# Kernel optimization log

Hardware: AMD Instinct MI355X
Metric: run time of the kernel (lower is better)

Reference implementation:

```python
import jax, jax.numpy as jnp
import numpy as np

OUT = 128
TYPES = [("author", 100000, 128), ("paper", 250000, 256), ("venue", 25000, 64),
         ("institution", 50000, 128), ("field", 75000, 64), ("term", 150000, 128)]


def setup_inputs() -> dict:
    key = jax.random.key(0)
    inp = {}
    for i, (name, n, f_in) in enumerate(TYPES):
        kx, kw, kb = jax.random.split(jax.random.fold_in(key, i), 3)
        inp[f"x_{name}"] = jax.random.normal(kx, (n, f_in), dtype=jnp.float32)
        # kaiming_uniform default init of torch Linear: bound = 1/sqrt(fan_in)
        bound = 1.0 / np.sqrt(f_in)
        inp[f"W_{name}"] = jax.random.uniform(kw, (OUT, f_in), dtype=jnp.float32, minval=-bound, maxval=bound)
        inp[f"b_{name}"] = jax.random.uniform(kb, (OUT,), dtype=jnp.float32, minval=-bound, maxval=bound)
    return inp


def reference(x_author, x_paper, x_venue, x_institution, x_field, x_term,
              W_author, b_author, W_paper, b_paper, W_venue, b_venue,
              W_institution, b_institution, W_field, b_field, W_term, b_term):
    # Per-type independent Linear: y_k = x_k @ W_k^T + b_k (grouped GEMM)
    def lin(x, W, b):
        return jnp.einsum('nf,of->no', x, W) + b
    return (lin(x_author, W_author, b_author),
            lin(x_paper, W_paper, b_paper),
            lin(x_venue, W_venue, b_venue),
            lin(x_institution, W_institution, b_institution),
            lin(x_field, W_field, b_field),
            lin(x_term, W_term, b_term))
```

## Files before the change

kernel.cpp:

```cpp
#include <hip/hip_runtime.h>

typedef __bf16 bf16x4 __attribute__((ext_vector_type(4)));
typedef __bf16 bf16x8 __attribute__((ext_vector_type(8)));
typedef float  f32x4  __attribute__((ext_vector_type(4)));

struct KArgs {
    const float* x[6];
    const float* W[6];
    const float* b[6];
    float*       out[6];
    int nrows[6];
    int blk0[7];
};

template<int FIN>
__device__ __forceinline__ void run_type(
    const float* __restrict__ x, const float* __restrict__ W,
    const float* __restrict__ bias, float* __restrict__ out,
    int nrows, int c0, int c1, __bf16* __restrict__ Alds)
{
    constexpr int KS    = (FIN < 128) ? FIN : 128;
    constexpr int NSLAB = FIN / KS;
    constexpr int NC    = FIN / 32;
    constexpr int CPS   = KS / 32;
    constexpr int UPT   = KS / 16;
    constexpr int BATCH = (UPT > 4) ? 4 : UPT;

    const int tid  = threadIdx.x;
    const int lane = tid & 63;
    const int wave = tid >> 6;
    const int l15  = lane & 15;
    const int lq   = lane >> 4;

    bf16x8 Wf[NC][2];
    f32x4  bv[2];
    #pragma unroll
    for (int t = 0; t < 2; ++t) {
        const int o = wave * 32 + t * 16 + l15;
        #pragma unroll
        for (int c = 0; c < NC; ++c) {
            const int k0 = c * 32 + lq * 8;
            const f32x4 w0 = *(const f32x4*)(W + (size_t)o * FIN + k0);
            const f32x4 w1 = *(const f32x4*)(W + (size_t)o * FIN + k0 + 4);
            bf16x8 f;
            f[0] = (__bf16)w0[0]; f[1] = (__bf16)w0[1];
            f[2] = (__bf16)w0[2]; f[3] = (__bf16)w0[3];
            f[4] = (__bf16)w1[0]; f[5] = (__bf16)w1[1];
            f[6] = (__bf16)w1[2]; f[7] = (__bf16)w1[3];
            Wf[c][t] = f;
        }
        bv[t] = *(const f32x4*)(bias + wave * 32 + t * 16 + lq * 4);
    }

    for (int chunk = c0; chunk < c1; ++chunk) {
        const int row0 = chunk * 64;
        f32x4 acc[4][2] = {};

        #pragma unroll
        for (int slab = 0; slab < NSLAB; ++slab) {
            __syncthreads();

            #pragma unroll
            for (int b0 = 0; b0 < UPT; b0 += BATCH) {
                f32x4 tmp[BATCH];
                #pragma unroll
                for (int i = 0; i < BATCH; ++i) {
                    const int u  = tid + (b0 + i) * 256;
                    const int r  = u / (KS / 4);
                    const int kq = u % (KS / 4);
                    int gr = row0 + r;
                    if (gr >= nrows) gr = nrows - 1;
                    tmp[i] = __builtin_nontemporal_load(
                        (const f32x4*)(x + (size_t)gr * FIN + slab * KS + kq * 4));
                }
                #pragma unroll
                for (int i = 0; i < BATCH; ++i) {
                    const int u  = tid + (b0 + i) * 256;
                    const int r  = u / (KS / 4);
                    const int kq = u % (KS / 4);
                    bf16x4 bq;
                    bq[0] = (__bf16)tmp[i][0]; bq[1] = (__bf16)tmp[i][1];
                    bq[2] = (__bf16)tmp[i][2]; bq[3] = (__bf16)tmp[i][3];
                    const int byte = (r * KS * 2 + kq * 8) ^ ((r & 7) << 4);
                    *(bf16x4*)((char*)Alds + byte) = bq;
                }
            }
            __syncthreads();

            #pragma unroll
            for (int nt = 0; nt < 4; ++nt) {
                const int row = nt * 16 + l15;
                #pragma unroll
                for (int c = 0; c < CPS; ++c) {
                    const int byte = (row * KS * 2 + c * 64 + lq * 16) ^ ((row & 7) << 4);
                    const bf16x8 xf = *(const bf16x8*)((char*)Alds + byte);
                    acc[nt][0] = __builtin_amdgcn_mfma_f32_16x16x32_bf16(
                        Wf[slab * CPS + c][0], xf, acc[nt][0], 0, 0, 0);
                    acc[nt][1] = __builtin_amdgcn_mfma_f32_16x16x32_bf16(
                        Wf[slab * CPS + c][1], xf, acc[nt][1], 0, 0, 0);
                }
            }
        }

        #pragma unroll
        for (int nt = 0; nt < 4; ++nt) {
            const int xrow = row0 + nt * 16 + l15;
            if (xrow < nrows) {
                #pragma unroll
                for (int t = 0; t < 2; ++t) {
                    const f32x4 v = acc[nt][t] + bv[t];
                    __builtin_nontemporal_store(v,
                        (f32x4*)(out + (size_t)xrow * 128 + wave * 32 + t * 16 + lq * 4));
                }
            }
        }
    }
}

__global__ __launch_bounds__(256) void hetero_fused_kern(KArgs A)
{
    __shared__ __bf16 Alds[64 * 128];

    int ty = 0;
    const int bid = blockIdx.x;
    while (ty < 5 && bid >= A.blk0[ty + 1]) ++ty;
    const int lb = bid - A.blk0[ty];
    const int nb = A.blk0[ty + 1] - A.blk0[ty];

    const int nrows  = A.nrows[ty];
    const int chunks = (nrows + 63) >> 6;
    const int c0 = (int)(((long)chunks * lb) / nb);
    const int c1 = (int)(((long)chunks * (lb + 1)) / nb);
    if (c0 >= c1) return;

    switch (ty) {
        case 0: run_type<128>(A.x[0], A.W[0], A.b[0], A.out[0], nrows, c0, c1, Alds); break;
        case 1: run_type<256>(A.x[1], A.W[1], A.b[1], A.out[1], nrows, c0, c1, Alds); break;
        case 2: run_type< 64>(A.x[2], A.W[2], A.b[2], A.out[2], nrows, c0, c1, Alds); break;
        case 3: run_type<128>(A.x[3], A.W[3], A.b[3], A.out[3], nrows, c0, c1, Alds); break;
        case 4: run_type< 64>(A.x[4], A.W[4], A.b[4], A.out[4], nrows, c0, c1, Alds); break;
        case 5: run_type<128>(A.x[5], A.W[5], A.b[5], A.out[5], nrows, c0, c1, Alds); break;
    }
}

extern "C" void kernel_launch(void* const* d_in, const int* in_sizes, int n_in,
                              void* d_out, int out_size, void* d_ws, size_t ws_size,
                              hipStream_t stream)
{
    float* out = (float*)d_out;
    KArgs A;
    const int   nrows[6] = {100000, 250000, 25000, 50000, 75000, 150000};
    const long  ooff[6]  = {0L, 12800000L, 44800000L, 48000000L, 54400000L, 64000000L};
    const int   blk0[7]  = {0, 273, 1297, 1348, 1485, 1639, 2048};
    for (int t = 0; t < 6; ++t) {
        A.x[t]     = (const float*)d_in[3 * t + 0];
        A.W[t]     = (const float*)d_in[3 * t + 1];
        A.b[t]     = (const float*)d_in[3 * t + 2];
        A.out[t]   = out + ooff[t];
        A.nrows[t] = nrows[t];
    }
    for (int i = 0; i < 7; ++i) A.blk0[i] = blk0[i];

    hetero_fused_kern<<<2048, 256, 0, stream>>>(A);
}
```

Baseline: 169.2 us.

## Load activations directly into MFMA fragments, dropping LDS staging and barriers

Replaces the shared-memory staging of activation tiles with direct per-lane global loads converted straight into bf16 MFMA operands, removing both __syncthreads per slab. Each wave now covers 16 rows by 64 output columns, so a block handles 32-row chunks and every weight fragment set doubles in registers. This aims to cut LDS traffic and barrier stalls and to add an occupancy hint. In exchange, each x row is fetched by two waves, global access is less coalesced per instruction, and register pressure rises for the 256-wide type.

```diff
diff --git a/kernel.cpp b/kernel.cpp
--- a/kernel.cpp
+++ b/kernel.cpp
@@ -1,6 +1,5 @@
 #include <hip/hip_runtime.h>
 
-typedef __bf16 bf16x4 __attribute__((ext_vector_type(4)));
 typedef __bf16 bf16x8 __attribute__((ext_vector_type(8)));
 typedef float  f32x4  __attribute__((ext_vector_type(4)));
 
@@ -17,31 +16,26 @@
 __device__ __forceinline__ void run_type(
     const float* __restrict__ x, const float* __restrict__ W,
     const float* __restrict__ bias, float* __restrict__ out,
-    int nrows, int c0, int c1, __bf16* __restrict__ Alds)
+    int nrows, int c0, int c1)
 {
-    constexpr int KS    = (FIN < 128) ? FIN : 128;
-    constexpr int NSLAB = FIN / KS;
-    constexpr int NC    = FIN / 32;
-    constexpr int CPS   = KS / 32;
-    constexpr int UPT   = KS / 16;
-    constexpr int BATCH = (UPT > 4) ? 4 : UPT;
+    constexpr int NC = FIN / 32;
 
-    const int tid  = threadIdx.x;
-    const int lane = tid & 63;
-    const int wave = tid >> 6;
-    const int l15  = lane & 15;
-    const int lq   = lane >> 4;
+    const int tid     = threadIdx.x;
+    const int lane    = tid & 63;
+    const int wave    = tid >> 6;
+    const int l15     = lane & 15;
+    const int lq      = lane >> 4;
+    const int rowgrp  = wave >> 1;
+    const int colbase = (wave & 1) * 64;
 
-    bf16x8 Wf[NC][2];
-    f32x4  bv[2];
+    bf16x8 Wf[NC][4];
     #pragma unroll
-    for (int t = 0; t < 2; ++t) {
-        const int o = wave * 32 + t * 16 + l15;
+    for (int t = 0; t < 4; ++t) {
+        const int o = colbase + t * 16 + l15;
         #pragma unroll
         for (int c = 0; c < NC; ++c) {
-            const int k0 = c * 32 + lq * 8;
-            const f32x4 w0 = *(const f32x4*)(W + (size_t)o * FIN + k0);
-            const f32x4 w1 = *(const f32x4*)(W + (size_t)o * FIN + k0 + 4);
+            const f32x4 w0 = *(const f32x4*)(W + (size_t)o * FIN + c * 32 + lq * 8);
+            const f32x4 w1 = *(const f32x4*)(W + (size_t)o * FIN + c * 32 + lq * 8 + 4);
             bf16x8 f;
             f[0] = (__bf16)w0[0]; f[1] = (__bf16)w0[1];
             f[2] = (__bf16)w0[2]; f[3] = (__bf16)w0[3];
@@ -49,78 +43,44 @@
             f[6] = (__bf16)w1[2]; f[7] = (__bf16)w1[3];
             Wf[c][t] = f;
         }
-        bv[t] = *(const f32x4*)(bias + wave * 32 + t * 16 + lq * 4);
     }
+    f32x4 bv[4];
+    #pragma unroll
+    for (int t = 0; t < 4; ++t)
+        bv[t] = *(const f32x4*)(bias + colbase + t * 16 + lq * 4);
 
     for (int chunk = c0; chunk < c1; ++chunk) {
-        const int row0 = chunk * 64;
-        f32x4 acc[4][2] = {};
+        const int xrow = chunk * 32 + rowgrp * 16 + l15;
+        const int gr   = (xrow < nrows) ? xrow : (nrows - 1);
+        const float* xp = x + (size_t)gr * FIN;
 
+        f32x4 acc[4] = {};
         #pragma unroll
-        for (int slab = 0; slab < NSLAB; ++slab) {
-            __syncthreads();
-
-            #pragma unroll
-            for (int b0 = 0; b0 < UPT; b0 += BATCH) {
-                f32x4 tmp[BATCH];
-                #pragma unroll
-                for (int i = 0; i < BATCH; ++i) {
-                    const int u  = tid + (b0 + i) * 256;
-                    const int r  = u / (KS / 4);
-                    const int kq = u % (KS / 4);
-                    int gr = row0 + r;
-                    if (gr >= nrows) gr = nrows - 1;
-                    tmp[i] = __builtin_nontemporal_load(
-                        (const f32x4*)(x + (size_t)gr * FIN + slab * KS + kq * 4));
-                }
-                #pragma unroll
-                for (int i = 0; i < BATCH; ++i) {
-                    const int u  = tid + (b0 + i) * 256;
-                    const int r  = u / (KS / 4);
-                    const int kq = u % (KS / 4);
-                    bf16x4 bq;
-                    bq[0] = (__bf16)tmp[i][0]; bq[1] = (__bf16)tmp[i][1];
-                    bq[2] = (__bf16)tmp[i][2]; bq[3] = (__bf16)tmp[i][3];
-                    const int byte = (r * KS * 2 + kq * 8) ^ ((r & 7) << 4);
-                    *(bf16x4*)((char*)Alds + byte) = bq;
-                }
-            }
-            __syncthreads();
-
-            #pragma unroll
-            for (int nt = 0; nt < 4; ++nt) {
-                const int row = nt * 16 + l15;
-                #pragma unroll
-                for (int c = 0; c < CPS; ++c) {
-                    const int byte = (row * KS * 2 + c * 64 + lq * 16) ^ ((row & 7) << 4);
-                    const bf16x8 xf = *(const bf16x8*)((char*)Alds + byte);
-                    acc[nt][0] = __builtin_amdgcn_mfma_f32_16x16x32_bf16(
-                        Wf[slab * CPS + c][0], xf, acc[nt][0], 0, 0, 0);
-                    acc[nt][1] = __builtin_amdgcn_mfma_f32_16x16x32_bf16(
-                        Wf[slab * CPS + c][1], xf, acc[nt][1], 0, 0, 0);
-                }
-            }
+        for (int c = 0; c < NC; ++c) {
+            const f32x4 v0 = __builtin_nontemporal_load((const f32x4*)(xp + c * 32 + lq * 8));
+            const f32x4 v1 = __builtin_nontemporal_load((const f32x4*)(xp + c * 32 + lq * 8 + 4));
+            bf16x8 xc;
+            xc[0] = (__bf16)v0[0]; xc[1] = (__bf16)v0[1];
+            xc[2] = (__bf16)v0[2]; xc[3] = (__bf16)v0[3];
+            xc[4] = (__bf16)v1[0]; xc[5] = (__bf16)v1[1];
+            xc[6] = (__bf16)v1[2]; xc[7] = (__bf16)v1[3];
+            acc[0] = __builtin_amdgcn_mfma_f32_16x16x32_bf16(Wf[c][0], xc, acc[0], 0, 0, 0);
+            acc[1] = __builtin_amdgcn_mfma_f32_16x16x32_bf16(Wf[c][1], xc, acc[1], 0, 0, 0);
+            acc[2] = __builtin_amdgcn_mfma_f32_16x16x32_bf16(Wf[c][2], xc, acc[2], 0, 0, 0);
+            acc[3] = __builtin_amdgcn_mfma_f32_16x16x32_bf16(Wf[c][3], xc, acc[3], 0, 0, 0);
         }
 
-        #pragma unroll
-        for (int nt = 0; nt < 4; ++nt) {
-            const int xrow = row0 + nt * 16 + l15;
-            if (xrow < nrows) {
-                #pragma unroll
-                for (int t = 0; t < 2; ++t) {
-                    const f32x4 v = acc[nt][t] + bv[t];
-                    __builtin_nontemporal_store(v,
-                        (f32x4*)(out + (size_t)xrow * 128 + wave * 32 + t * 16 + lq * 4));
-                }
-            }
+        if (xrow < nrows) {
+            float* op = out + (size_t)xrow * 128 + colbase;
+            #pragma unroll
+            for (int t = 0; t < 4; ++t)
+                __builtin_nontemporal_store(acc[t] + bv[t], (f32x4*)(op + t * 16 + lq * 4));
         }
     }
 }
 
-__global__ __launch_bounds__(256) void hetero_fused_kern(KArgs A)
+__global__ __launch_bounds__(256, 2) void hetero_fused_kern(KArgs A)
 {
-    __shared__ __bf16 Alds[64 * 128];
-
     int ty = 0;
     const int bid = blockIdx.x;
     while (ty < 5 && bid >= A.blk0[ty + 1]) ++ty;
@@ -128,18 +88,18 @@
     const int nb = A.blk0[ty + 1] - A.blk0[ty];
 
     const int nrows  = A.nrows[ty];
-    const int chunks = (nrows + 63) >> 6;
+    const int chunks = (nrows + 31) >> 5;
     const int c0 = (int)(((long)chunks * lb) / nb);
     const int c1 = (int)(((long)chunks * (lb + 1)) / nb);
     if (c0 >= c1) return;
 
     switch (ty) {
-        case 0: run_type<128>(A.x[0], A.W[0], A.b[0], A.out[0], nrows, c0, c1, Alds); break;
-        case 1: run_type<256>(A.x[1], A.W[1], A.b[1], A.out[1], nrows, c0, c1, Alds); break;
-        case 2: run_type< 64>(A.x[2], A.W[2], A.b[2], A.out[2], nrows, c0, c1, Alds); break;
-        case 3: run_type<128>(A.x[3], A.W[3], A.b[3], A.out[3], nrows, c0, c1, Alds); break;
-        case 4: run_type< 64>(A.x[4], A.W[4], A.b[4], A.out[4], nrows, c0, c1, Alds); break;
-        case 5: run_type<128>(A.x[5], A.W[5], A.b[5], A.out[5], nrows, c0, c1, Alds); break;
+        case 0: run_type<128>(A.x[0], A.W[0], A.b[0], A.out[0], nrows, c0, c1); break;
+        case 1: run_type<256>(A.x[1], A.W[1], A.b[1], A.out[1], nrows, c0, c1); break;
+        case 2: run_type< 64>(A.x[2], A.W[2], A.b[2], A.out[2], nrows, c0, c1); break;
+        case 3: run_type<128>(A.x[3], A.W[3], A.b[3], A.out[3], nrows, c0, c1); break;
+        case 4: run_type< 64>(A.x[4], A.W[4], A.b[4], A.out[4], nrows, c0, c1); break;
+        case 5: run_type<128>(A.x[5], A.W[5], A.b[5], A.out[5], nrows, c0, c1); break;
     }
 }
 
@@ -149,9 +109,9 @@
 {
     float* out = (float*)d_out;
     KArgs A;
-    const int   nrows[6] = {100000, 250000, 25000, 50000, 75000, 150000};
-    const long  ooff[6]  = {0L, 12800000L, 44800000L, 48000000L, 54400000L, 64000000L};
-    const int   blk0[7]  = {0, 273, 1297, 1348, 1485, 1639, 2048};
+    const int  nrows[6] = {100000, 250000, 25000, 50000, 75000, 150000};
+    const long ooff[6]  = {0L, 12800000L, 44800000L, 48000000L, 54400000L, 64000000L};
+    const int  blk0[7]  = {0, 273, 1297, 1348, 1485, 1639, 2048};
     for (int t = 0; t < 6; ++t) {
         A.x[t]     = (const float*)d_in[3 * t + 0];
         A.W[t]     = (const float*)d_in[3 * t + 1];
```

Result: slower. 273.2 us (+61.4%).
